# Performance work log

Measured on AMD Instinct MI355X. Metric: run time of the kernel, lower is better.

The kernel has to match this reference:

```python
import jax, jax.numpy as jnp
import numpy as np

NUM_HEADS = 8
NUM_POINTS = 4


def setup_inputs() -> dict:
    key = jax.random.key(0)
    ks = jax.random.split(key, 10)
    B, H, W, D = 8, 64, 64, 256
    N = H * W
    nh, P = NUM_HEADS, NUM_POINTS

    def xavier(k, shape):
        fan_in, fan_out = shape[0], shape[1]
        lim = float(np.sqrt(6.0 / (fan_in + fan_out)))
        return jax.random.uniform(k, shape, jnp.float32, -lim, lim)

    x = jax.random.normal(ks[0], (B, N, D), jnp.float32)
    qkv_w = xavier(ks[1], (D, 3 * D))
    qkv_b = jnp.zeros((3 * D,), jnp.float32)
    # offset network is zero-init in the module; use small random weights so the
    # deformable sampling is actually exercised (offsets nonzero).
    off_w = jax.random.normal(ks[2], (D, nh * P * 2), jnp.float32) * 0.01
    off_b = jnp.zeros((nh * P * 2,), jnp.float32)
    attw_w = xavier(ks[3], (D, nh * P))
    attw_b = jnp.zeros((nh * P,), jnp.float32)
    proj_w = xavier(ks[4], (D, D))
    proj_b = jnp.zeros((D,), jnp.float32)
    return {
        "x": x, "qkv_w": qkv_w, "qkv_b": qkv_b,
        "off_w": off_w, "off_b": off_b,
        "attw_w": attw_w, "attw_b": attw_b,
        "proj_w": proj_w, "proj_b": proj_b,
        "H": 64, "W": 64,
    }


def _deformable_forward(x, qkv_w, qkv_b, off_w, off_b, attw_w, attw_b, proj_w, proj_b, H, W):
    B, N, D = x.shape
    nh, P = NUM_HEADS, NUM_POINTS
    hd = D // nh

    qkv = x @ qkv_w + qkv_b                      # [B,N,3D] (q,k computed but unused, as in the original)
    v = qkv[..., 2 * D:].reshape(B, N, nh, hd)   # [B,N,nh,hd]

    offsets = jnp.tanh((x @ off_w + off_b).reshape(B, N, nh, P, 2)) * 2.0

    ys, xs = jnp.meshgrid(jnp.arange(H, dtype=x.dtype), jnp.arange(W, dtype=x.dtype), indexing="ij")
    ref = jnp.stack([xs, ys], axis=-1).reshape(N, 2)          # [N,2] (x,y) pixel coords
    loc = ref[None, :, None, None, :] + offsets               # [B,N,nh,P,2] pixel coords
    # (module normalizes to [-1,1] then grid_sample align_corners=True un-normalizes
    #  back to exactly these pixel coordinates, so we sample at `loc` directly)

    # value as flat spatial map per head: [B,nh,hd,N], n = y*W + x
    vf = v.transpose(0, 2, 3, 1).reshape(B, nh, hd, N)

    gx, gy = loc[..., 0], loc[..., 1]
    x0 = jnp.floor(gx); y0 = jnp.floor(gy)
    x1 = x0 + 1.0;      y1 = y0 + 1.0
    wx1 = gx - x0; wx0 = 1.0 - wx1
    wy1 = gy - y0; wy0 = 1.0 - wy1

    def corner(xi, yi, w):
        # bilinear corner with zeros padding: zero weight if corner out of bounds
        valid = (xi >= 0) & (xi < W) & (yi >= 0) & (yi < H)
        idx = (jnp.clip(yi, 0, H - 1) * W + jnp.clip(xi, 0, W - 1)).astype(jnp.int32)
        idx2 = idx.transpose(0, 2, 1, 3).reshape(B, nh, N * P)          # [B,nh,N*P]
        g = jnp.take_along_axis(vf, idx2[:, :, None, :], axis=3)        # [B,nh,hd,N*P]
        w2 = (w * valid.astype(x.dtype)).transpose(0, 2, 1, 3).reshape(B, nh, 1, N * P)
        return g * w2

    sampled = (corner(x0, y0, wx0 * wy0) + corner(x1, y0, wx1 * wy0)
               + corner(x0, y1, wx0 * wy1) + corner(x1, y1, wx1 * wy1))
    sampled = sampled.reshape(B, nh, hd, N, P)

    attn = jax.nn.softmax((x @ attw_w + attw_b).reshape(B, N, nh, P), axis=-1)
    out = jnp.einsum("bhcnp,bnhp->bnhc", sampled, attn).reshape(B, N, D)
    return out @ proj_w + proj_b


def reference(x, qkv_w, qkv_b, off_w, off_b, attw_w, attw_b, proj_w, proj_b, H, W):
    return _deformable_forward(x, qkv_w, qkv_b, off_w, off_b, attw_w, attw_b, proj_w, proj_b, H, W)
```

## Files before the change

kernel.cpp:

```cpp
#include <hip/hip_runtime.h>
#include <hip/hip_bf16.h>
#include <cmath>

#define NN 4096
typedef __attribute__((ext_vector_type(8))) short short8;
typedef __attribute__((ext_vector_type(4))) float f32x4;

__device__ __forceinline__ float bf2f(unsigned short u) {
  union { unsigned int i; float f; } c; c.i = ((unsigned int)u) << 16; return c.f;
}

__global__ __launch_bounds__(256) void cvt_w(
    const float* __restrict__ qkv_w, const float* __restrict__ off_w,
    const float* __restrict__ attw_w, const float* __restrict__ proj_w,
    __hip_bfloat16* __restrict__ wcatT, __hip_bfloat16* __restrict__ pjT)
{
  const int t = threadIdx.x;
  if (blockIdx.x < 256) {
    int k = blockIdx.x;
    wcatT[t * 256 + k] = __float2bfloat16(qkv_w[k * 768 + 512 + t]);
    if (t < 128) {
      int c2 = 256 + t;
      float v = 0.f;
      if (c2 < 320)      v = off_w[k * 64 + (c2 - 256)];
      else if (c2 < 352) v = attw_w[k * 32 + (c2 - 320)];
      wcatT[c2 * 256 + k] = __float2bfloat16(v);
    }
  } else {
    int k = blockIdx.x - 256;
    pjT[t * 256 + k] = __float2bfloat16(proj_w[k * 256 + t]);
  }
}

__global__ __launch_bounds__(512) void gemm_voff(
    const float* __restrict__ x,
    const __hip_bfloat16* __restrict__ wcatT,
    const float* __restrict__ vbias,
    const float* __restrict__ off_b, const float* __restrict__ attw_b,
    __hip_bfloat16* __restrict__ vb,
    unsigned int* __restrict__ table)
{
  __shared__ float smemf[12800];
  short* As = (short*)smemf;
  short* Bs = As + 128 * 40;
  float (*L)[100] = (float(*)[100])smemf;

  const int t = threadIdx.x;
  const int bid = blockIdx.x;
  const int m0 = (((bid & 7) << 5) | (bid >> 3)) * 128;
  const int wave = t >> 6, lane = t & 63, q = lane >> 4, ln = lane & 15;
  const int wm = (wave & 1) * 64, wn = (wave >> 1) * 96;

  f32x4 acc[4][6] = {};

  const int arow = t >> 2, aseg = t & 3;
  const float* apg = x + (size_t)(m0 + arow) * 256 + aseg * 8;

  for (int k0 = 0; k0 < 256; k0 += 32) {
    float4 f0 = *(const float4*)(apg + k0);
    float4 f1 = *(const float4*)(apg + k0 + 4);
    alignas(16) __hip_bfloat16 cv[8] = {
      __float2bfloat16(f0.x), __float2bfloat16(f0.y), __float2bfloat16(f0.z), __float2bfloat16(f0.w),
      __float2bfloat16(f1.x), __float2bfloat16(f1.y), __float2bfloat16(f1.z), __float2bfloat16(f1.w)};
    *(int4*)&As[arow * 40 + aseg * 8] = *(int4*)cv;
#pragma unroll
    for (int i = 0; i < 3; ++i) {
      int u = t + i * 512;
      int brow = u >> 2, bseg = u & 3;
      *(int4*)&Bs[brow * 40 + bseg * 8] =
          *(const int4*)&wcatT[(size_t)brow * 256 + k0 + bseg * 8];
    }
    __syncthreads();
    short8 a[4], b[6];
#pragma unroll
    for (int i = 0; i < 4; ++i) a[i] = *(const short8*)&As[(wm + i * 16 + ln) * 40 + q * 8];
#pragma unroll
    for (int j = 0; j < 6; ++j) b[j] = *(const short8*)&Bs[(wn + j * 16 + ln) * 40 + q * 8];
#pragma unroll
    for (int i = 0; i < 4; ++i)
#pragma unroll
      for (int j = 0; j < 6; ++j)
        acc[i][j] = __builtin_amdgcn_mfma_f32_16x16x32_bf16(a[i], b[j], acc[i][j], 0, 0, 0);
    __syncthreads();
  }

#pragma unroll
  for (int j = 0; j < 6; ++j) {
    int col = wn + j * 16 + ln;
    if (col < 256) {
      float bv = vbias[col];
#pragma unroll
      for (int i = 0; i < 4; ++i) {
        int rowb = m0 + wm + i * 16 + q * 4;
#pragma unroll
        for (int r = 0; r < 4; ++r)
          vb[(size_t)(rowb + r) * 256 + col] = __float2bfloat16(acc[i][j][r] + bv);
      }
    } else if (col < 352) {
      int lc = col - 256;
      float bv = (lc < 64) ? off_b[lc] : attw_b[lc - 64];
#pragma unroll
      for (int i = 0; i < 4; ++i)
#pragma unroll
        for (int r = 0; r < 4; ++r)
          L[wm + i * 16 + q * 4 + r][lc] = acc[i][j][r] + bv;
    }
  }
  __syncthreads();

#pragma unroll
  for (int it = 0; it < 2; ++it) {
    int pl = t + it * 512;
    int rr = pl >> 3, h = pl & 7;
    int row = m0 + rr;

    float a0 = L[rr][64 + h * 4 + 0], a1 = L[rr][64 + h * 4 + 1];
    float a2 = L[rr][64 + h * 4 + 2], a3 = L[rr][64 + h * 4 + 3];
    float mx = fmaxf(fmaxf(a0, a1), fmaxf(a2, a3));
    float e0 = expf(a0 - mx), e1 = expf(a1 - mx), e2 = expf(a2 - mx), e3 = expf(a3 - mx);
    float inv = 1.f / (e0 + e1 + e2 + e3);

    alignas(16) _Float16 pk[12];
#pragma unroll
    for (int p = 0; p < 4; ++p) {
      pk[p * 2 + 0] = (_Float16)(2.f * tanhf(L[rr][h * 8 + p * 2 + 0]));
      pk[p * 2 + 1] = (_Float16)(2.f * tanhf(L[rr][h * 8 + p * 2 + 1]));
    }
    pk[8]  = (_Float16)(e0 * inv);
    pk[9]  = (_Float16)(e1 * inv);
    pk[10] = (_Float16)(e2 * inv);
    pk[11] = (_Float16)(e3 * inv);

    size_t pg = (size_t)row * 8 + h;
    *(uint4*)(table + pg * 8)     = *(uint4*)&pk[0];
    *(uint2*)(table + pg * 8 + 4) = *(uint2*)&pk[8];
  }
}

__global__ __launch_bounds__(256) void sample_kernel(
    const __hip_bfloat16* __restrict__ v,
    const unsigned int* __restrict__ table,
    __hip_bfloat16* __restrict__ y)
{
  __shared__ uint4 Tab[128];
  const int t = threadIdx.x;
  const int bid = blockIdx.x;
  const int p0 = (((bid & 7) << 9) | (bid >> 3)) * 64;
  if (t < 128) Tab[t] = *(const uint4*)(table + (size_t)p0 * 8 + t * 4);
  __syncthreads();

  const int g = t & 3, p = t >> 2;
  const int pg = p0 + p;
  const int h = pg & 7;
  const int row = pg >> 3;
  const int b = row >> 12;
  const int nl = row & (NN - 1);
  const float refx = (float)(nl & 63);
  const float refy = (float)(nl >> 6);

  const _Float16* dp  = (const _Float16*)&Tab[p * 2];
  const _Float16* ap_ = (const _Float16*)&Tab[p * 2 + 1];

  alignas(16) unsigned short idxs[16];
  float ws[16];
#pragma unroll
  for (int pp = 0; pp < 4; ++pp) {
    float gx = refx + (float)dp[2 * pp + 0];
    float gy = refy + (float)dp[2 * pp + 1];
    float x0f = floorf(gx), y0f = floorf(gy);
    int x0 = (int)x0f, y0 = (int)y0f;
    int x1 = x0 + 1,   y1 = y0 + 1;
    float wx1 = gx - x0f, wx0 = 1.f - wx1;
    float wy1 = gy - y0f, wy0 = 1.f - wy1;
    int cx0 = min(max(x0, 0), 63), cx1 = min(max(x1, 0), 63);
    int cy0 = min(max(y0, 0), 63), cy1 = min(max(y1, 0), 63);
    float vx0 = (x0 >= 0 && x0 <= 63) ? 1.f : 0.f;
    float vx1 = (x1 >= 0 && x1 <= 63) ? 1.f : 0.f;
    float vy0 = (y0 >= 0 && y0 <= 63) ? 1.f : 0.f;
    float vy1 = (y1 >= 0 && y1 <= 63) ? 1.f : 0.f;
    float apv = (float)ap_[pp];
    idxs[pp * 4 + 0] = (unsigned short)(cy0 * 64 + cx0);
    idxs[pp * 4 + 1] = (unsigned short)(cy0 * 64 + cx1);
    idxs[pp * 4 + 2] = (unsigned short)(cy1 * 64 + cx0);
    idxs[pp * 4 + 3] = (unsigned short)(cy1 * 64 + cx1);
    ws[pp * 4 + 0] = apv * wx0 * wy0 * vx0 * vy0;
    ws[pp * 4 + 1] = apv * wx1 * wy0 * vx1 * vy0;
    ws[pp * 4 + 2] = apv * wx0 * wy1 * vx0 * vy1;
    ws[pp * 4 + 3] = apv * wx1 * wy1 * vx1 * vy1;
  }

  const char* vbase = (const char*)(v + (size_t)b * NN * 256 + h * 32 + g * 8);

  float acc[8] = {};
#pragma unroll
  for (int j = 0; j < 16; ++j) {
    float w = ws[j];
    int idx = idxs[j];
    int4 pk = *(const int4*)(vbase + (size_t)idx * 512);
    const unsigned short* u = (const unsigned short*)&pk;
#pragma unroll
    for (int c = 0; c < 8; ++c) acc[c] += w * bf2f(u[c]);
  }
  alignas(16) __hip_bfloat16 o[8];
#pragma unroll
  for (int c = 0; c < 8; ++c) o[c] = __float2bfloat16(acc[c]);
  *(int4*)((char*)y + ((size_t)row * 256 + h * 32 + g * 8) * 2) = *(int4*)o;
}

__global__ __launch_bounds__(256) void gemm_proj(
    const short* __restrict__ A, const short* __restrict__ BT,
    const float* __restrict__ bias, float* __restrict__ out)
{
  __shared__ short As[64 * 40];
  __shared__ short Bs[256 * 40];
  const int t = threadIdx.x;
  const int bid = blockIdx.x;
  const int m0 = (((bid & 7) << 6) | (bid >> 3)) * 64;
  const int wave = t >> 6, lane = t & 63, q = lane >> 4, ln = lane & 15;
  const int wn = wave * 64;

  f32x4 acc[4][4] = {};

  const int arow = t >> 2, aseg = t & 3;
  const short* apg = A + (size_t)(m0 + arow) * 256 + aseg * 8;

  for (int k0 = 0; k0 < 256; k0 += 32) {
    *(int4*)&As[arow * 40 + aseg * 8] = *(const int4*)(apg + k0);
#pragma unroll
    for (int u2 = 0; u2 < 4; ++u2) {
      int c = t + u2 * 256;
      int col = c >> 2, kq = c & 3;
      *(int4*)&Bs[col * 40 + kq * 8] =
          *(const int4*)&BT[(size_t)col * 256 + k0 + kq * 8];
    }
    __syncthreads();
    short8 a[4], b[4];
#pragma unroll
    for (int i = 0; i < 4; ++i) a[i] = *(const short8*)&As[(i * 16 + ln) * 40 + q * 8];
#pragma unroll
    for (int j = 0; j < 4; ++j) b[j] = *(const short8*)&Bs[(wn + j * 16 + ln) * 40 + q * 8];
#pragma unroll
    for (int i = 0; i < 4; ++i)
#pragma unroll
      for (int j = 0; j < 4; ++j)
        acc[i][j] = __builtin_amdgcn_mfma_f32_16x16x32_bf16(a[i], b[j], acc[i][j], 0, 0, 0);
    __syncthreads();
  }

#pragma unroll
  for (int j = 0; j < 4; ++j) {
    int col = wn + j * 16 + ln;
    float bv = bias[col];
#pragma unroll
    for (int i = 0; i < 4; ++i) {
      int rowb = m0 + i * 16 + q * 4;
#pragma unroll
      for (int r = 0; r < 4; ++r)
        out[(size_t)(rowb + r) * 256 + col] = acc[i][j][r] + bv;
    }
  }
}

extern "C" void kernel_launch(void* const* d_in, const int* in_sizes, int n_in,
                              void* d_out, int out_size, void* d_ws, size_t ws_size,
                              hipStream_t stream) {
  const float* x      = (const float*)d_in[0];
  const float* qkv_w  = (const float*)d_in[1];
  const float* qkv_b  = (const float*)d_in[2];
  const float* off_w  = (const float*)d_in[3];
  const float* off_b  = (const float*)d_in[4];
  const float* attw_w = (const float*)d_in[5];
  const float* attw_b = (const float*)d_in[6];
  const float* proj_w = (const float*)d_in[7];
  const float* proj_b = (const float*)d_in[8];
  float* out = (float*)d_out;

  char* ws = (char*)d_ws;
  __hip_bfloat16* vb    = (__hip_bfloat16*)(ws);
  __hip_bfloat16* yb    = (__hip_bfloat16*)(ws + 16777216);
  unsigned int*   table = (unsigned int*)  (ws + 33554432);
  __hip_bfloat16* wcatT = (__hip_bfloat16*)(ws + 41943040);
  __hip_bfloat16* pjT   = (__hip_bfloat16*)(ws + 42139648);

  cvt_w<<<512, 256, 0, stream>>>(qkv_w, off_w, attw_w, proj_w, wcatT, pjT);
  gemm_voff<<<256, 512, 0, stream>>>(x, wcatT, qkv_b + 512, off_b, attw_b, vb, table);
  sample_kernel<<<4096, 256, 0, stream>>>(vb, table, yb);
  gemm_proj<<<512, 256, 0, stream>>>((const short*)yb, (const short*)pjT, proj_b, out);
}
```

Measured before the change: 142.5 us.

## Double-buffer LDS tiles in fused V/offset GEMM with register prefetch

Restructures the k-loop of the fused projection GEMM so that global loads for the next K tile are issued into registers before the MFMAs of the current tile. After the MFMAs they are written into a second LDS buffer, which drops one barrier per iteration. This is meant to hide global-memory latency behind matrix math. In exchange it uses more LDS (two A/B buffers) and more registers, which may lower occupancy.

```diff
diff --git a/kernel.cpp b/kernel.cpp
--- a/kernel.cpp
+++ b/kernel.cpp
@@ -40,10 +40,8 @@
     __hip_bfloat16* __restrict__ vb,
     unsigned int* __restrict__ table)
 {
-  __shared__ float smemf[12800];
-  short* As = (short*)smemf;
-  short* Bs = As + 128 * 40;
-  float (*L)[100] = (float(*)[100])smemf;
+  __shared__ short smem[40960];
+  float (*L)[100] = (float(*)[100])smem;
 
   const int t = threadIdx.x;
   const int bid = blockIdx.x;
@@ -55,22 +53,43 @@
 
   const int arow = t >> 2, aseg = t & 3;
   const float* apg = x + (size_t)(m0 + arow) * 256 + aseg * 8;
-
+  const int adst = arow * 40 + aseg * 8;
+
+  int bdst[3];
+  const __hip_bfloat16* bsrc[3];
+#pragma unroll
+  for (int i = 0; i < 3; ++i) {
+    int u = t + i * 512, brow = u >> 2, bseg = u & 3;
+    bdst[i] = brow * 40 + bseg * 8;
+    bsrc[i] = wcatT + (size_t)brow * 256 + bseg * 8;
+  }
+
+  float4 fa0 = *(const float4*)(apg);
+  float4 fa1 = *(const float4*)(apg + 4);
+  int4 br[3];
+#pragma unroll
+  for (int i = 0; i < 3; ++i) br[i] = *(const int4*)(bsrc[i]);
+  {
+    alignas(16) __hip_bfloat16 cv[8] = {
+      __float2bfloat16(fa0.x), __float2bfloat16(fa0.y), __float2bfloat16(fa0.z), __float2bfloat16(fa0.w),
+      __float2bfloat16(fa1.x), __float2bfloat16(fa1.y), __float2bfloat16(fa1.z), __float2bfloat16(fa1.w)};
+    *(int4*)&smem[adst] = *(int4*)cv;
+#pragma unroll
+    for (int i = 0; i < 3; ++i) *(int4*)&smem[5120 + bdst[i]] = br[i];
+  }
+  __syncthreads();
+
+  int cur = 0;
   for (int k0 = 0; k0 < 256; k0 += 32) {
-    float4 f0 = *(const float4*)(apg + k0);
-    float4 f1 = *(const float4*)(apg + k0 + 4);
-    alignas(16) __hip_bfloat16 cv[8] = {
-      __float2bfloat16(f0.x), __float2bfloat16(f0.y), __float2bfloat16(f0.z), __float2bfloat16(f0.w),
-      __float2bfloat16(f1.x), __float2bfloat16(f1.y), __float2bfloat16(f1.z), __float2bfloat16(f1.w)};
-    *(int4*)&As[arow * 40 + aseg * 8] = *(int4*)cv;
-#pragma unroll
-    for (int i = 0; i < 3; ++i) {
-      int u = t + i * 512;
-      int brow = u >> 2, bseg = u & 3;
-      *(int4*)&Bs[brow * 40 + bseg * 8] =
-          *(const int4*)&wcatT[(size_t)brow * 256 + k0 + bseg * 8];
-    }
-    __syncthreads();
+    const bool haveNext = (k0 < 224);
+    if (haveNext) {
+      fa0 = *(const float4*)(apg + k0 + 32);
+      fa1 = *(const float4*)(apg + k0 + 36);
+#pragma unroll
+      for (int i = 0; i < 3; ++i) br[i] = *(const int4*)(bsrc[i] + k0 + 32);
+    }
+    const short* As = smem + cur * 20480;
+    const short* Bs = As + 5120;
     short8 a[4], b[6];
 #pragma unroll
     for (int i = 0; i < 4; ++i) a[i] = *(const short8*)&As[(wm + i * 16 + ln) * 40 + q * 8];
@@ -81,7 +100,18 @@
 #pragma unroll
       for (int j = 0; j < 6; ++j)
         acc[i][j] = __builtin_amdgcn_mfma_f32_16x16x32_bf16(a[i], b[j], acc[i][j], 0, 0, 0);
+    if (haveNext) {
+      short* An = smem + (cur ^ 1) * 20480;
+      short* Bn = An + 5120;
+      alignas(16) __hip_bfloat16 cv[8] = {
+        __float2bfloat16(fa0.x), __float2bfloat16(fa0.y), __float2bfloat16(fa0.z), __float2bfloat16(fa0.w),
+        __float2bfloat16(fa1.x), __float2bfloat16(fa1.y), __float2bfloat16(fa1.z), __float2bfloat16(fa1.w)};
+      *(int4*)&An[adst] = *(int4*)cv;
+#pragma unroll
+      for (int i = 0; i < 3; ++i) *(int4*)&Bn[bdst[i]] = br[i];
+    }
     __syncthreads();
+    cur ^= 1;
   }
 
 #pragma unroll
```

Result: no change. 143.1 us (+0.4%).
